# Performance work log

Hardware: AMD Instinct MI355X
Metric: run time of the kernel (lower is better)

The kernel has to match this reference:

```python
import jax, jax.numpy as jnp
import numpy as np

# perm_inv_n with comps = [
#   [[0],[0]]        -> einsum 'Zab->Zb'            (row-sum, prepro eliminates single axis-a)
#   [[0,0],[0,1]]    -> einsum 'Zab,Zac->Zbc'       (Gram matrix over axis a)
#   [[0,0],[0,0]]    -> einsum 'Zab,Zab->Zb'        (column sum of squares)
#   [[0,1],[0,0]]    -> prepro 'Zab->Zb' twice, then 'Zb,Zb->Zb' (squared column sums)
#   [[0,0,1],[0,1,2]]-> prepro arg2 'Zab->Zd', then 'Zab,Zac,Zd->Zbcd' (Gram x colsum outer)
# ] and sz=[512,64]. Outputs are flattened per-Z and concatenated (order = comps order).

def setup_inputs() -> dict:
    key = jax.random.key(0)
    x = jax.random.normal(key, (256, 512, 64), dtype=jnp.float32)
    return {"x": x}

def reference(x) -> jnp.ndarray:
    Z = x.shape[0]
    cs = jnp.sum(x, axis=1)                       # [Z, b]   'Zab->Zb'
    gram = jnp.einsum('zab,zac->zbc', x, x)       # [Z, b, b]
    h1 = cs                                       # comp 0
    h2 = gram.reshape(Z, -1)                      # comp 1
    h3 = jnp.einsum('zab,zab->zb', x, x)          # comp 2
    h4 = cs * cs                                  # comp 3
    h5 = (gram[:, :, :, None] * cs[:, None, None, :]).reshape(Z, -1)  # comp 4: 'Zbc,Zd->Zbcd'
    return jnp.concatenate([h1, h2, h3, h4, h5], axis=-1)  # [Z, 64+4096+64+64+262144]
```

## Files before the change

kernel.cpp:

```cpp
#include <hip/hip_runtime.h>

#define Z_DIM 256
#define A_DIM 512
#define B_DIM 64
#define PER_Z 266432
#define GRAM_OFF 64
#define H3_OFF 4160
#define H4_OFF 4224
#define H5_OFF 4288
#define CHUNK 128

__global__ __launch_bounds__(256) void k_stats(const float* __restrict__ x,
                                               float* __restrict__ out) {
    __shared__ float sx[CHUNK * B_DIM];
    const int z = blockIdx.x;
    const int t = threadIdx.x;
    const float* xz = x + (size_t)z * (A_DIM * B_DIM);
    float* oz = out + (size_t)z * PER_Z;

    const int tb = t >> 4;
    const int tc = t & 15;

    float acc[4][4];
#pragma unroll
    for (int i = 0; i < 4; i++)
#pragma unroll
        for (int j = 0; j < 4; j++) acc[i][j] = 0.f;

    float cs_acc = 0.f, ss_acc = 0.f;

    for (int a0 = 0; a0 < A_DIM; a0 += CHUNK) {
        const float4* src = (const float4*)(xz + a0 * B_DIM);
        float4* dst = (float4*)sx;
#pragma unroll
        for (int i = 0; i < 8; i++) dst[t + i * 256] = src[t + i * 256];
        __syncthreads();

        for (int a = 0; a < CHUNK; a++) {
            float4 bv = *(const float4*)&sx[a * B_DIM + tb * 4];
            float4 cv = *(const float4*)&sx[a * B_DIM + tc * 4];
            float bb[4] = {bv.x, bv.y, bv.z, bv.w};
            float cc[4] = {cv.x, cv.y, cv.z, cv.w};
#pragma unroll
            for (int i = 0; i < 4; i++)
#pragma unroll
                for (int j = 0; j < 4; j++)
                    acc[i][j] = fmaf(bb[i], cc[j], acc[i][j]);
        }

        if (t < B_DIM) {
#pragma unroll 4
            for (int a = 0; a < CHUNK; a++) {
                float v = sx[a * B_DIM + t];
                cs_acc += v;
                ss_acc = fmaf(v, v, ss_acc);
            }
        }
        __syncthreads();
    }

#pragma unroll
    for (int i = 0; i < 4; i++) {
        float4 v = make_float4(acc[i][0], acc[i][1], acc[i][2], acc[i][3]);
        *(float4*)&oz[GRAM_OFF + (size_t)(tb * 4 + i) * B_DIM + tc * 4] = v;
    }
    if (t < B_DIM) {
        oz[t] = cs_acc;
        oz[H3_OFF + t] = ss_acc;
        oz[H4_OFF + t] = cs_acc * cs_acc;
    }
}

__global__ __launch_bounds__(256) void k_outer(float* __restrict__ out) {
    const int z = blockIdx.x >> 6;
    const int s = blockIdx.x & 63;
    const int t = threadIdx.x;
    float* oz = out + (size_t)z * PER_Z;
    const float* gram = oz + GRAM_OFF;
    const float* cs = oz;
    float4* o5 = (float4*)(oz + H5_OFF);
#pragma unroll
    for (int i = 0; i < 4; i++) {
        int q = s * 1024 + i * 256 + t;
        int bc = q >> 4;
        int dg = q & 15;
        float g = gram[bc];
        float4 c4 = *(const float4*)&cs[dg * 4];
        o5[q] = make_float4(g * c4.x, g * c4.y, g * c4.z, g * c4.w);
    }
}

extern "C" void kernel_launch(void* const* d_in, const int* in_sizes, int n_in,
                              void* d_out, int out_size, void* d_ws, size_t ws_size,
                              hipStream_t stream) {
    const float* x = (const float*)d_in[0];
    float* out = (float*)d_out;
    k_stats<<<Z_DIM, 256, 0, stream>>>(x, out);
    k_outer<<<Z_DIM * 64, 256, 0, stream>>>(out);
}
```

Measured before the change: 319.2 us.

## Fuse stats and outer-product kernels, split A across two half-blocks

Merges the Gram/colsum kernel and the outer-product kernel into one kernel of 512 threads per Z. Two halves each process alternate A chunks and reduce their partial Gram sums through shared memory. The column sum of squares is taken from the Gram diagonal, and the large H5 output is written from shared memory with nontemporal stores. This removes a launch and the global reread of gram/cs. The cost is only 256 blocks writing about 270MB, which may limit memory-level parallelism compared with 16K blocks.

```diff
diff --git a/kernel.cpp b/kernel.cpp
--- a/kernel.cpp
+++ b/kernel.cpp
@@ -10,35 +10,45 @@
 #define H5_OFF 4288
 #define CHUNK 128
 
-__global__ __launch_bounds__(256) void k_stats(const float* __restrict__ x,
+typedef float f4v __attribute__((ext_vector_type(4)));
+
+__global__ __launch_bounds__(512) void k_fused(const float* __restrict__ x,
                                                float* __restrict__ out) {
-    __shared__ float sx[CHUNK * B_DIM];
+    __shared__ float sx[2][CHUNK * B_DIM];
+    __shared__ float sg[B_DIM * B_DIM];
+    __shared__ float scs1[B_DIM];
+    __shared__ float scs[B_DIM];
+
     const int z = blockIdx.x;
     const int t = threadIdx.x;
+    const int half = t >> 8;
+    const int u = t & 255;
+    const int tb = u >> 4;
+    const int tc = u & 15;
+
     const float* xz = x + (size_t)z * (A_DIM * B_DIM);
     float* oz = out + (size_t)z * PER_Z;
-
-    const int tb = t >> 4;
-    const int tc = t & 15;
 
     float acc[4][4];
 #pragma unroll
     for (int i = 0; i < 4; i++)
 #pragma unroll
         for (int j = 0; j < 4; j++) acc[i][j] = 0.f;
+    float cs_acc = 0.f;
 
-    float cs_acc = 0.f, ss_acc = 0.f;
+    float* my_sx = sx[half];
 
-    for (int a0 = 0; a0 < A_DIM; a0 += CHUNK) {
+    for (int c = 0; c < 2; c++) {
+        const int a0 = (c * 2 + half) * CHUNK;
         const float4* src = (const float4*)(xz + a0 * B_DIM);
-        float4* dst = (float4*)sx;
+        float4* dst = (float4*)my_sx;
 #pragma unroll
-        for (int i = 0; i < 8; i++) dst[t + i * 256] = src[t + i * 256];
+        for (int i = 0; i < 8; i++) dst[u + i * 256] = src[u + i * 256];
         __syncthreads();
 
         for (int a = 0; a < CHUNK; a++) {
-            float4 bv = *(const float4*)&sx[a * B_DIM + tb * 4];
-            float4 cv = *(const float4*)&sx[a * B_DIM + tc * 4];
+            float4 bv = *(const float4*)&my_sx[a * B_DIM + tb * 4];
+            float4 cv = *(const float4*)&my_sx[a * B_DIM + tc * 4];
             float bb[4] = {bv.x, bv.y, bv.z, bv.w};
             float cc[4] = {cv.x, cv.y, cv.z, cv.w};
 #pragma unroll
@@ -47,46 +57,51 @@
                 for (int j = 0; j < 4; j++)
                     acc[i][j] = fmaf(bb[i], cc[j], acc[i][j]);
         }
-
-        if (t < B_DIM) {
+        if (u < B_DIM) {
 #pragma unroll 4
-            for (int a = 0; a < CHUNK; a++) {
-                float v = sx[a * B_DIM + t];
-                cs_acc += v;
-                ss_acc = fmaf(v, v, ss_acc);
-            }
+            for (int a = 0; a < CHUNK; a++) cs_acc += my_sx[a * B_DIM + u];
         }
         __syncthreads();
     }
 
+    if (half) {
 #pragma unroll
-    for (int i = 0; i < 4; i++) {
-        float4 v = make_float4(acc[i][0], acc[i][1], acc[i][2], acc[i][3]);
-        *(float4*)&oz[GRAM_OFF + (size_t)(tb * 4 + i) * B_DIM + tc * 4] = v;
+        for (int i = 0; i < 4; i++) {
+            float4 v = make_float4(acc[i][0], acc[i][1], acc[i][2], acc[i][3]);
+            *(float4*)&sg[(tb * 4 + i) * B_DIM + tc * 4] = v;
+        }
+        if (u < B_DIM) scs1[u] = cs_acc;
     }
-    if (t < B_DIM) {
-        oz[t] = cs_acc;
-        oz[H3_OFF + t] = ss_acc;
-        oz[H4_OFF + t] = cs_acc * cs_acc;
+    __syncthreads();
+    if (!half) {
+#pragma unroll
+        for (int i = 0; i < 4; i++) {
+            float4 p = *(const float4*)&sg[(tb * 4 + i) * B_DIM + tc * 4];
+            float4 v = make_float4(acc[i][0] + p.x, acc[i][1] + p.y,
+                                   acc[i][2] + p.z, acc[i][3] + p.w);
+            *(float4*)&sg[(tb * 4 + i) * B_DIM + tc * 4] = v;
+            *(float4*)&oz[GRAM_OFF + (size_t)(tb * 4 + i) * B_DIM + tc * 4] = v;
+        }
+        if (u < B_DIM) {
+            float c = cs_acc + scs1[u];
+            scs[u] = c;
+            oz[u] = c;
+            oz[H4_OFF + u] = c * c;
+        }
     }
-}
+    __syncthreads();
+    if (!half && u < B_DIM) oz[H3_OFF + u] = sg[u * B_DIM + u];
 
-__global__ __launch_bounds__(256) void k_outer(float* __restrict__ out) {
-    const int z = blockIdx.x >> 6;
-    const int s = blockIdx.x & 63;
-    const int t = threadIdx.x;
-    float* oz = out + (size_t)z * PER_Z;
-    const float* gram = oz + GRAM_OFF;
-    const float* cs = oz;
-    float4* o5 = (float4*)(oz + H5_OFF);
-#pragma unroll
-    for (int i = 0; i < 4; i++) {
-        int q = s * 1024 + i * 256 + t;
+    f4v* o5 = (f4v*)(oz + H5_OFF);
+#pragma unroll 4
+    for (int i = 0; i < 128; i++) {
+        int q = i * 512 + t;
         int bc = q >> 4;
         int dg = q & 15;
-        float g = gram[bc];
-        float4 c4 = *(const float4*)&cs[dg * 4];
-        o5[q] = make_float4(g * c4.x, g * c4.y, g * c4.z, g * c4.w);
+        float g = sg[bc];
+        const float* c4 = &scs[dg * 4];
+        f4v v = {g * c4[0], g * c4[1], g * c4[2], g * c4[3]};
+        __builtin_nontemporal_store(v, &o5[q]);
     }
 }
 
@@ -95,6 +110,5 @@
                               hipStream_t stream) {
     const float* x = (const float*)d_in[0];
     float* out = (float*)d_out;
-    k_stats<<<Z_DIM, 256, 0, stream>>>(x, out);
-    k_outer<<<Z_DIM * 64, 256, 0, stream>>>(out);
+    k_fused<<<Z_DIM, 512, 0, stream>>>(x, out);
 }
```

Measured after the change: 308.8 us. -3.3%, faster.
